# Performance work log

Measured on AMD Instinct MI355X. Metric: run time of the kernel, lower is better.

## Reference

```python
import jax, jax.numpy as jnp
import numpy as np

NUM_EMBEDDINGS = 512
EMBEDDING_DIM = 256
COMMITMENT_COST = 0.25


def setup_inputs() -> dict:
    key = jax.random.key(0)
    k1, k2 = jax.random.split(key)
    z = jax.random.normal(k1, (8, EMBEDDING_DIM, 16, 32, 32), dtype=jnp.float32)
    # codebook initialized uniform(-1/K, 1/K) like the torch module
    e = jax.random.uniform(k2, (NUM_EMBEDDINGS, EMBEDDING_DIM), dtype=jnp.float32,
                           minval=-1.0 / NUM_EMBEDDINGS, maxval=1.0 / NUM_EMBEDDINGS)
    return {"z": z, "e": e}


def reference(z, e):
    B, D, T, h, w = z.shape
    K = e.shape[0]
    # [B,D,T,h,w] -> [N, D]
    z_flat = jnp.transpose(z, (0, 2, 3, 4, 1)).reshape(-1, D)
    # squared L2 distances to codebook: [N, K]
    d = (jnp.sum(z_flat ** 2, axis=1, keepdims=True)
         + jnp.sum(e ** 2, axis=1)
         - 2.0 * z_flat @ e.T)
    idx = jnp.argmin(d, axis=1)                      # [N] int
    z_q_raw = e[idx].reshape(B, T, h, w, D)          # codebook gather
    z_q_raw = jnp.transpose(z_q_raw, (0, 4, 1, 2, 3))  # [B,D,T,h,w]

    commit = jnp.mean((jax.lax.stop_gradient(z_q_raw) - z) ** 2)
    codebk = jnp.mean((z_q_raw - jax.lax.stop_gradient(z)) ** 2)
    vq_loss = codebk + COMMITMENT_COST * commit

    # straight-through estimator
    z_q = z + jax.lax.stop_gradient(z_q_raw - z)

    # perplexity: histogram of code usage (avoids materializing NxK one-hot)
    N = idx.shape[0]
    avg_probs = jnp.zeros((K,), z.dtype).at[idx].add(1.0) / N
    perplexity = jnp.exp(-jnp.sum(avg_probs * jnp.log(avg_probs + 1e-10)))

    return z_q, vq_loss, idx, perplexity
```

## Files before the change

kernel.cpp:

```cpp
#include <hip/hip_runtime.h>
#include <math.h>

#define N_POS     131072
#define DIM       256
#define K_CODES   512
#define S_SPATIAL 16384
#define ZQ_ELEMS  33554432
#define OUT_LOSS  33554432
#define OUT_IDXB  33554433
#define OUT_PERP  (33554433 + 131072)

#define WS_LOSS   0
#define WS_HIST   16
#define WS_E2     2064
#define WS_FIXED  2064

__global__ __launch_bounds__(256) void e2_kernel(const float* __restrict__ e,
                                                 float* __restrict__ e2) {
    int k = blockIdx.x * 256 + threadIdx.x;
    if (k >= K_CODES) return;
    const float* row = e + (size_t)k * DIM;
    float half[2];
#pragma unroll
    for (int h = 0; h < 2; ++h) {
        const float* base = row + h * 128;
        float r[8];
#pragma unroll
        for (int j = 0; j < 8; ++j) {
            float v = base[j];
            r[j] = __fmul_rn(v, v);
        }
        for (int i = 8; i < 128; i += 8) {
#pragma unroll
            for (int j = 0; j < 8; ++j) {
                float v = base[i + j];
                r[j] = __fadd_rn(r[j], __fmul_rn(v, v));
            }
        }
        half[h] = __fadd_rn(__fadd_rn(__fadd_rn(r[0], r[1]), __fadd_rn(r[2], r[3])),
                            __fadd_rn(__fadd_rn(r[4], r[5]), __fadd_rn(r[6], r[7])));
    }
    e2[k] = __fadd_rn(half[0], half[1]);
}

__global__ __launch_bounds__(256) void transpose_e(const float* __restrict__ e,
                                                   float* __restrict__ eTp) {
    int t = blockIdx.x * 256 + threadIdx.x;
    int k = t >> 8;
    int d = t & 255;
    float v = e[t];
    int w = k >> 7;
    int c = (k >> 6) & 1;
    int l = k & 63;
    eTp[d * K_CODES + (w << 7) + (l << 1) + c] = v;
}

__global__ __launch_bounds__(256) void sz_kernel(const float* __restrict__ z,
                                                 float* __restrict__ sz) {
    int n = blockIdx.x * 256 + threadIdx.x;
    int b = n >> 14;
    int s = n & (S_SPATIAL - 1);
    const float* zp = z + (size_t)b * (DIM * S_SPATIAL) + s;
    float half[2];
#pragma unroll
    for (int h = 0; h < 2; ++h) {
        const float* base = zp + (size_t)(h * 128) * S_SPATIAL;
        float r[8];
#pragma unroll
        for (int j = 0; j < 8; ++j) {
            float v = base[(size_t)j * S_SPATIAL];
            r[j] = __fmul_rn(v, v);
        }
        for (int i = 8; i < 128; i += 8) {
#pragma unroll
            for (int j = 0; j < 8; ++j) {
                float v = base[(size_t)(i + j) * S_SPATIAL];
                r[j] = __fadd_rn(r[j], __fmul_rn(v, v));
            }
        }
        half[h] = __fadd_rn(__fadd_rn(__fadd_rn(r[0], r[1]), __fadd_rn(r[2], r[3])),
                            __fadd_rn(__fadd_rn(r[4], r[5]), __fadd_rn(r[6], r[7])));
    }
    sz[n] = __fadd_rn(half[0], half[1]);
}

__global__ __launch_bounds__(256) void pass1_dist(const float* __restrict__ z,
                                                  const float* __restrict__ eTp,
                                                  const float* __restrict__ e2,
                                                  const float* __restrict__ sz,
                                                  float* __restrict__ idxf) {
    const int lane = threadIdx.x & 63;
    const int wave = threadIdx.x >> 6;
    const int n0   = blockIdx.x << 4;
    const int b    = n0 >> 14;
    const float* zb = z + (size_t)b * (DIM * S_SPATIAL) + (n0 & (S_SPATIAL - 1));

    __shared__ float zs[DIM][16];
    __shared__ unsigned long long lred[4][16];

    for (int j = threadIdx.x; j < 1024; j += 256) {
        int d  = j >> 2;
        int p4 = (j & 3) << 2;
        float4 v = *(const float4*)(zb + ((size_t)d << 14) + p4);
        *(float4*)(&zs[d][p4]) = v;
    }

    float szv = sz[n0 + (lane & 15)];

    const int k0 = (wave << 7) + lane;
    float se0 = e2[k0];
    float se1 = e2[k0 + 64];

    float acc0[16], acc1[16];
#pragma unroll
    for (int p = 0; p < 16; ++p) { acc0[p] = 0.f; acc1[p] = 0.f; }

    __syncthreads();

    const float* ep = eTp + (wave << 7) + (lane << 1);
#pragma unroll 2
    for (int d = 0; d < DIM; ++d) {
        float2 ev = *(const float2*)(ep + (size_t)d * K_CODES);
        float zv[16];
        *(float4*)(zv +  0) = *(const float4*)(&zs[d][ 0]);
        *(float4*)(zv +  4) = *(const float4*)(&zs[d][ 4]);
        *(float4*)(zv +  8) = *(const float4*)(&zs[d][ 8]);
        *(float4*)(zv + 12) = *(const float4*)(&zs[d][12]);
#pragma unroll
        for (int p = 0; p < 16; ++p) {
            acc0[p] = __fmaf_rn(zv[p], ev.x, acc0[p]);
            acc1[p] = __fmaf_rn(zv[p], ev.y, acc1[p]);
        }
    }

#pragma unroll
    for (int p = 0; p < 16; ++p) {
        float szp = __shfl(szv, p);
        float d0 = __fsub_rn(__fadd_rn(szp, se0), __fmul_rn(2.0f, acc0[p]));
        float d1 = __fsub_rn(__fadd_rn(szp, se1), __fmul_rn(2.0f, acc1[p]));
        unsigned long long key0 =
            ((unsigned long long)__float_as_uint(d0) << 32) | (unsigned int)k0;
        unsigned long long key1 =
            ((unsigned long long)__float_as_uint(d1) << 32) | (unsigned int)(k0 + 64);
        unsigned long long kmin = key1 < key0 ? key1 : key0;
#pragma unroll
        for (int off = 32; off; off >>= 1) {
            unsigned long long o = __shfl_xor(kmin, off);
            kmin = o < kmin ? o : kmin;
        }
        if (lane == 0) lred[wave][p] = kmin;
    }
    __syncthreads();
    if (threadIdx.x < 16) {
        int p = threadIdx.x;
        unsigned long long m01 = lred[0][p] < lred[1][p] ? lred[0][p] : lred[1][p];
        unsigned long long m23 = lred[2][p] < lred[3][p] ? lred[2][p] : lred[3][p];
        unsigned long long m   = m01 < m23 ? m01 : m23;
        idxf[n0 + p] = (float)(unsigned int)(m & 0xffffffffull);
    }
}

__global__ __launch_bounds__(256) void hist_kernel(const float* __restrict__ idxf,
                                                   int* __restrict__ ghist) {
    __shared__ int h[K_CODES];
    for (int k = threadIdx.x; k < K_CODES; k += 256) h[k] = 0;
    __syncthreads();
    int n = blockIdx.x * 256 + threadIdx.x;
    int idx = (int)idxf[n];
    atomicAdd(&h[idx], 1);
    __syncthreads();
    for (int k = threadIdx.x; k < K_CODES; k += 256) {
        int c = h[k];
        if (c) atomicAdd(&ghist[k], c);
    }
}

__global__ __launch_bounds__(256) void gather_loss(const float* __restrict__ z,
                                                   const float* __restrict__ e,
                                                   const float* __restrict__ idxf,
                                                   float* __restrict__ out,
                                                   double* __restrict__ loss) {
    int t = blockIdx.x * 256 + threadIdx.x;
    int b   = t >> 14;
    int r   = t & 16383;
    int dg  = r >> 12;
    int sp  = (r & 4095) << 2;
    int n0  = (b << 14) + sp;

    int k0 = (int)idxf[n0 + 0];
    int k1 = (int)idxf[n0 + 1];
    int k2 = (int)idxf[n0 + 2];
    int k3 = (int)idxf[n0 + 3];
    const float* e0 = e + (size_t)k0 * DIM;
    const float* e1 = e + (size_t)k1 * DIM;
    const float* e2p = e + (size_t)k2 * DIM;
    const float* e3 = e + (size_t)k3 * DIM;

    const float* zb = z + ((size_t)b * DIM << 14) + sp;
    float* ob = out + ((size_t)b * DIM << 14) + sp;

    double acc = 0.0;
    int dend = dg * 64 + 64;
    for (int d0 = dg * 64; d0 < dend; d0 += 4) {
        float4 ev0 = *(const float4*)(e0 + d0);
        float4 ev1 = *(const float4*)(e1 + d0);
        float4 ev2 = *(const float4*)(e2p + d0);
        float4 ev3 = *(const float4*)(e3 + d0);
#pragma unroll
        for (int dd = 0; dd < 4; ++dd) {
            size_t off = ((size_t)(d0 + dd) << 14);
            float4 zv = *(const float4*)(zb + off);
            float ea = (dd == 0) ? ev0.x : (dd == 1) ? ev0.y : (dd == 2) ? ev0.z : ev0.w;
            float eb_ = (dd == 0) ? ev1.x : (dd == 1) ? ev1.y : (dd == 2) ? ev1.z : ev1.w;
            float ec = (dd == 0) ? ev2.x : (dd == 1) ? ev2.y : (dd == 2) ? ev2.z : ev2.w;
            float ed = (dd == 0) ? ev3.x : (dd == 1) ? ev3.y : (dd == 2) ? ev3.z : ev3.w;
            float d0f = __fsub_rn(ea, zv.x);
            float d1f = __fsub_rn(eb_, zv.y);
            float d2f = __fsub_rn(ec, zv.z);
            float d3f = __fsub_rn(ed, zv.w);
            float4 ov;
            ov.x = __fadd_rn(zv.x, d0f);
            ov.y = __fadd_rn(zv.y, d1f);
            ov.z = __fadd_rn(zv.z, d2f);
            ov.w = __fadd_rn(zv.w, d3f);
            *(float4*)(ob + off) = ov;
            acc += (double)d0f * (double)d0f;
            acc += (double)d1f * (double)d1f;
            acc += (double)d2f * (double)d2f;
            acc += (double)d3f * (double)d3f;
        }
    }
    for (int off = 32; off; off >>= 1) acc += __shfl_down(acc, off);
    __shared__ double red[4];
    if ((threadIdx.x & 63) == 0) red[threadIdx.x >> 6] = acc;
    __syncthreads();
    if (threadIdx.x == 0) {
        double tsum = red[0] + red[1] + red[2] + red[3];
        atomicAdd(loss, tsum);
    }
}

__global__ __launch_bounds__(512) void finalize_kernel(const int* __restrict__ ghist,
                                                       const double* __restrict__ loss,
                                                       float* __restrict__ out) {
    int k = threadIdx.x;
    double p = (double)ghist[k] / (double)N_POS;
    double t = p * log(p + 1e-10);
    for (int off = 32; off; off >>= 1) t += __shfl_down(t, off);
    __shared__ double red[8];
    if ((k & 63) == 0) red[k >> 6] = t;
    __syncthreads();
    if (k == 0) {
        double sum = 0.0;
        for (int i = 0; i < 8; ++i) sum += red[i];
        double perp = exp(-sum);
        double mse  = (*loss) / (double)ZQ_ELEMS;
        out[OUT_LOSS] = (float)(1.25 * mse);
        out[OUT_PERP] = (float)perp;
    }
}

extern "C" void kernel_launch(void* const* d_in, const int* in_sizes, int n_in,
                              void* d_out, int out_size, void* d_ws, size_t ws_size,
                              hipStream_t stream) {
    const float* z = (const float*)d_in[0];
    const float* e = (const float*)d_in[1];
    float* out = (float*)d_out;
    char* ws = (char*)d_ws;

    double* loss  = (double*)(ws + WS_LOSS);
    int*    ghist = (int*)(ws + WS_HIST);
    float*  e2    = (float*)(ws + WS_E2);
    float*  idxf  = out + OUT_IDXB;

    float* eTp = (float*)d_out;
    float* szp = (float*)d_out + 131072;

    hipMemsetAsync(d_ws, 0, WS_FIXED, stream);

    e2_kernel      <<<2, 256, 0, stream>>>(e, e2);
    transpose_e    <<<512, 256, 0, stream>>>(e, eTp);
    sz_kernel      <<<N_POS / 256, 256, 0, stream>>>(z, szp);
    pass1_dist     <<<N_POS / 16, 256, 0, stream>>>(z, eTp, e2, szp, idxf);
    hist_kernel    <<<N_POS / 256, 256, 0, stream>>>(idxf, ghist);
    gather_loss    <<<N_POS / 256, 256, 0, stream>>>(z, e, idxf, out, loss);
    finalize_kernel<<<1, 512, 0, stream>>>(ghist, loss, out);
}
```

Before: 735.6 us.

## Widen per-thread code tile to four and fuse histogram into distance kernel

The distance kernel now runs 128 threads per block, and each thread accumulates four codebook columns instead of two. The codebook is re-laid out so each thread reads one float4 per dimension, which raises FMA work per shared-memory z load and halves the block-level reduction. The separate histogram kernel is removed, and each winning index is atomically added to the global histogram directly, trading one launch for more global atomics. Register pressure doubles for the accumulators, which may lower occupancy.

```diff
diff --git a/kernel.cpp b/kernel.cpp
--- a/kernel.cpp
+++ b/kernel.cpp
@@ -44,15 +44,15 @@
 }
 
 __global__ __launch_bounds__(256) void transpose_e(const float* __restrict__ e,
-                                                   float* __restrict__ eTp) {
+                                                   float* __restrict__ eTq) {
     int t = blockIdx.x * 256 + threadIdx.x;
     int k = t >> 8;
     int d = t & 255;
     float v = e[t];
-    int w = k >> 7;
-    int c = (k >> 6) & 1;
+    int c = k >> 7;
+    int w = (k >> 6) & 1;
     int l = k & 63;
-    eTp[d * K_CODES + (w << 7) + (l << 1) + c] = v;
+    eTq[(((d << 1) + w) << 8) + (l << 2) + c] = v;
 }
 
 __global__ __launch_bounds__(256) void sz_kernel(const float* __restrict__ z,
@@ -84,11 +84,12 @@
     sz[n] = __fadd_rn(half[0], half[1]);
 }
 
-__global__ __launch_bounds__(256) void pass1_dist(const float* __restrict__ z,
-                                                  const float* __restrict__ eTp,
-                                                  const float* __restrict__ e2,
-                                                  const float* __restrict__ sz,
-                                                  float* __restrict__ idxf) {
+__global__ __launch_bounds__(128, 4) void pass1_dist(const float* __restrict__ z,
+                                                     const float* __restrict__ eTq,
+                                                     const float* __restrict__ e2,
+                                                     const float* __restrict__ sz,
+                                                     float* __restrict__ idxf,
+                                                     int* __restrict__ ghist) {
     const int lane = threadIdx.x & 63;
     const int wave = threadIdx.x >> 6;
     const int n0   = blockIdx.x << 4;
@@ -96,9 +97,9 @@
     const float* zb = z + (size_t)b * (DIM * S_SPATIAL) + (n0 & (S_SPATIAL - 1));
 
     __shared__ float zs[DIM][16];
-    __shared__ unsigned long long lred[4][16];
-
-    for (int j = threadIdx.x; j < 1024; j += 256) {
+    __shared__ unsigned long long lred[2][16];
+
+    for (int j = threadIdx.x; j < 1024; j += 128) {
         int d  = j >> 2;
         int p4 = (j & 3) << 2;
         float4 v = *(const float4*)(zb + ((size_t)d << 14) + p4);
@@ -107,20 +108,22 @@
 
     float szv = sz[n0 + (lane & 15)];
 
-    const int k0 = (wave << 7) + lane;
-    float se0 = e2[k0];
-    float se1 = e2[k0 + 64];
-
-    float acc0[16], acc1[16];
-#pragma unroll
-    for (int p = 0; p < 16; ++p) { acc0[p] = 0.f; acc1[p] = 0.f; }
-
-    __syncthreads();
-
-    const float* ep = eTp + (wave << 7) + (lane << 1);
+    const int kbase = (wave << 6) + lane;
+    float se0 = e2[kbase];
+    float se1 = e2[kbase + 128];
+    float se2 = e2[kbase + 256];
+    float se3 = e2[kbase + 384];
+
+    float a0[16], a1[16], a2[16], a3[16];
+#pragma unroll
+    for (int p = 0; p < 16; ++p) { a0[p] = 0.f; a1[p] = 0.f; a2[p] = 0.f; a3[p] = 0.f; }
+
+    __syncthreads();
+
+    const float* ep = eTq + (size_t)(((wave << 6) + lane) << 2);
 #pragma unroll 2
     for (int d = 0; d < DIM; ++d) {
-        float2 ev = *(const float2*)(ep + (size_t)d * K_CODES);
+        float4 ev = *(const float4*)(ep + ((size_t)d << 9));
         float zv[16];
         *(float4*)(zv +  0) = *(const float4*)(&zs[d][ 0]);
         *(float4*)(zv +  4) = *(const float4*)(&zs[d][ 4]);
@@ -128,21 +131,31 @@
         *(float4*)(zv + 12) = *(const float4*)(&zs[d][12]);
 #pragma unroll
         for (int p = 0; p < 16; ++p) {
-            acc0[p] = __fmaf_rn(zv[p], ev.x, acc0[p]);
-            acc1[p] = __fmaf_rn(zv[p], ev.y, acc1[p]);
+            a0[p] = __fmaf_rn(zv[p], ev.x, a0[p]);
+            a1[p] = __fmaf_rn(zv[p], ev.y, a1[p]);
+            a2[p] = __fmaf_rn(zv[p], ev.z, a2[p]);
+            a3[p] = __fmaf_rn(zv[p], ev.w, a3[p]);
         }
     }
 
 #pragma unroll
     for (int p = 0; p < 16; ++p) {
         float szp = __shfl(szv, p);
-        float d0 = __fsub_rn(__fadd_rn(szp, se0), __fmul_rn(2.0f, acc0[p]));
-        float d1 = __fsub_rn(__fadd_rn(szp, se1), __fmul_rn(2.0f, acc1[p]));
-        unsigned long long key0 =
-            ((unsigned long long)__float_as_uint(d0) << 32) | (unsigned int)k0;
-        unsigned long long key1 =
-            ((unsigned long long)__float_as_uint(d1) << 32) | (unsigned int)(k0 + 64);
-        unsigned long long kmin = key1 < key0 ? key1 : key0;
+        float d0 = __fsub_rn(__fadd_rn(szp, se0), __fmul_rn(2.0f, a0[p]));
+        float d1 = __fsub_rn(__fadd_rn(szp, se1), __fmul_rn(2.0f, a1[p]));
+        float d2 = __fsub_rn(__fadd_rn(szp, se2), __fmul_rn(2.0f, a2[p]));
+        float d3 = __fsub_rn(__fadd_rn(szp, se3), __fmul_rn(2.0f, a3[p]));
+        unsigned long long k0 =
+            ((unsigned long long)__float_as_uint(d0) << 32) | (unsigned int)(kbase);
+        unsigned long long k1 =
+            ((unsigned long long)__float_as_uint(d1) << 32) | (unsigned int)(kbase + 128);
+        unsigned long long k2 =
+            ((unsigned long long)__float_as_uint(d2) << 32) | (unsigned int)(kbase + 256);
+        unsigned long long k3 =
+            ((unsigned long long)__float_as_uint(d3) << 32) | (unsigned int)(kbase + 384);
+        unsigned long long m01 = k1 < k0 ? k1 : k0;
+        unsigned long long m23 = k3 < k2 ? k3 : k2;
+        unsigned long long kmin = m23 < m01 ? m23 : m01;
 #pragma unroll
         for (int off = 32; off; off >>= 1) {
             unsigned long long o = __shfl_xor(kmin, off);
@@ -153,25 +166,10 @@
     __syncthreads();
     if (threadIdx.x < 16) {
         int p = threadIdx.x;
-        unsigned long long m01 = lred[0][p] < lred[1][p] ? lred[0][p] : lred[1][p];
-        unsigned long long m23 = lred[2][p] < lred[3][p] ? lred[2][p] : lred[3][p];
-        unsigned long long m   = m01 < m23 ? m01 : m23;
-        idxf[n0 + p] = (float)(unsigned int)(m & 0xffffffffull);
-    }
-}
-
-__global__ __launch_bounds__(256) void hist_kernel(const float* __restrict__ idxf,
-                                                   int* __restrict__ ghist) {
-    __shared__ int h[K_CODES];
-    for (int k = threadIdx.x; k < K_CODES; k += 256) h[k] = 0;
-    __syncthreads();
-    int n = blockIdx.x * 256 + threadIdx.x;
-    int idx = (int)idxf[n];
-    atomicAdd(&h[idx], 1);
-    __syncthreads();
-    for (int k = threadIdx.x; k < K_CODES; k += 256) {
-        int c = h[k];
-        if (c) atomicAdd(&ghist[k], c);
+        unsigned long long m = lred[0][p] < lred[1][p] ? lred[0][p] : lred[1][p];
+        int idx = (int)(unsigned int)(m & 0xffffffffull);
+        idxf[n0 + p] = (float)idx;
+        atomicAdd(&ghist[idx], 1);
     }
 }
 
@@ -273,16 +271,15 @@
     float*  e2    = (float*)(ws + WS_E2);
     float*  idxf  = out + OUT_IDXB;
 
-    float* eTp = (float*)d_out;
+    float* eTq = (float*)d_out;
     float* szp = (float*)d_out + 131072;
 
     hipMemsetAsync(d_ws, 0, WS_FIXED, stream);
 
     e2_kernel      <<<2, 256, 0, stream>>>(e, e2);
-    transpose_e    <<<512, 256, 0, stream>>>(e, eTp);
+    transpose_e    <<<512, 256, 0, stream>>>(e, eTq);
     sz_kernel      <<<N_POS / 256, 256, 0, stream>>>(z, szp);
-    pass1_dist     <<<N_POS / 16, 256, 0, stream>>>(z, eTp, e2, szp, idxf);
-    hist_kernel    <<<N_POS / 256, 256, 0, stream>>>(idxf, ghist);
+    pass1_dist     <<<N_POS / 16, 128, 0, stream>>>(z, eTq, e2, szp, idxf, ghist);
     gather_loss    <<<N_POS / 256, 256, 0, stream>>>(z, e, idxf, out, loss);
     finalize_kernel<<<1, 512, 0, stream>>>(ghist, loss, out);
 }
```

Result: faster. 685.3 us (-6.8%).
